# Performance work log

Hardware: AMD Instinct MI355X
Metric: run time of the kernel (lower is better)

The kernel has to match this reference:

```python
import jax, jax.numpy as jnp
import numpy as np

S = 2048          # total tokens (prefill, batch folded into seq dim)
H = 32            # num query heads
HKV = 8           # num kv heads (GQA)
G = H // HKV      # query heads per kv head
D = 128           # head_dim
SCALE = D ** -0.5 # flex_attention default scale
DIFF_BS = 32      # diffusion block size for the block mask


def setup_inputs() -> dict:
    key = jax.random.key(0)
    k1, k2, k3 = jax.random.split(key, 3)
    q = jax.random.normal(k1, (S, H * D), dtype=jnp.float32)
    k = jax.random.normal(k2, (S, HKV * D), dtype=jnp.float32)
    v = jax.random.normal(k3, (S, HKV * D), dtype=jnp.float32)
    # diffusion block-causal mask: token i attends to all tokens in diffusion
    # blocks up to and including its own block (matches attn_metadata.block_mask
    # semantics fed into dllm_block_mask / flex_attention)
    blk = jnp.arange(S) // DIFF_BS
    block_mask = blk[:, None] >= blk[None, :]  # [S, S] bool
    return {"q": q, "k": k, "v": v, "block_mask": block_mask}


def reference(q, k, v, block_mask):
    # q: [S, H*D]; k, v: [S, HKV*D]; block_mask: [S, S] bool
    qh = q.reshape(S, HKV, G, D)   # group query heads by shared kv head (enable_gqa)
    kh = k.reshape(S, HKV, D)
    vh = v.reshape(S, HKV, D)
    # scores: [HKV, G, S_q, S_k]
    scores = jnp.einsum('qhgd,khd->hgqk', qh, kh) * SCALE
    neg = jnp.finfo(scores.dtype).min
    scores = jnp.where(block_mask[None, None, :, :], scores, neg)
    p = jax.nn.softmax(scores, axis=-1)
    o = jnp.einsum('hgqk,khd->qhgd', p, vh)  # [S, HKV, G, D]
    # prefill epilogue: rearrange '1 h s d -> s (h d)'
    return o.reshape(S, H * D)
```

## Files before the change

kernel.cpp:

```cpp
#include <hip/hip_runtime.h>
#include <hip/hip_bf16.h>

typedef __attribute__((ext_vector_type(8)))  short short8;
typedef __attribute__((ext_vector_type(16))) float f32x16;
typedef unsigned short u16;
typedef unsigned int   u32;

__device__ __forceinline__ u16 f2b(float f){
    __hip_bfloat16 h = __float2bfloat16(f);
    u16 u; __builtin_memcpy(&u, &h, 2); return u;
}
__device__ __forceinline__ u32 pk2(float lo, float hi){
    return (u32)f2b(lo) | ((u32)f2b(hi) << 16);
}
__device__ __forceinline__ float b2f(u16 u){
    u32 w = ((u32)u) << 16; float f; __builtin_memcpy(&f, &w, 4); return f;
}

#define PART_STRIDE 8448

template<bool SPLIT>
__global__ __launch_bounds__(256, 2)
void dllm_attn(const float* __restrict__ Qg, const float* __restrict__ Kg,
               const float* __restrict__ Vg, float* __restrict__ Og,
               char* __restrict__ Wg)
{
    __shared__ alignas(16) char kl[64 * 256];
    __shared__ alignas(16) char vl[128 * 128];

    const int bid = blockIdx.x;
    const int kh  = bid & 7;
    int tq, ci, uu = 0;
    if (SPLIT){
        uu = 159 - (bid >> 3);
        if (uu < 16)      { tq = uu; ci = 0; }
        else if (uu < 48) { const int x = uu - 16; tq = 16 + (x >> 1); ci = x & 1; }
        else if (uu < 96) { const int x = uu - 48; const int d3 = x / 3; tq = 32 + d3; ci = x - 3 * d3; }
        else              { const int x = uu - 96; tq = 48 + (x >> 2); ci = x & 3; }
    } else { tq = 63 - (bid >> 3); ci = 0; }
    const int q0   = tq << 5;
    const int nvis = q0 + 32;
    const int ntt  = (tq + 2) >> 1;
    const int t0   = SPLIT ? (ci << 3) : 0;
    const int t1   = SPLIT ? min(t0 + 8, ntt) : ntt;
    const int nch  = SPLIT ? ((tq >> 4) + 1) : 1;

    const int tid = threadIdx.x;
    const int wv  = tid >> 6;
    const int ln  = tid & 63;
    const int lq  = ln & 31;
    const int hi  = ln >> 5;
    const int swz = (ln & 7) << 4;
    const int h   = (kh << 2) + wv;

    const float QS = 0.088388347648318447f * 1.4426950408889634f;
    short8 qf[8];
    {
        const float* qp = Qg + (size_t)(q0 + lq) * 4096 + h * 128 + hi * 8;
        #pragma unroll
        for (int ds = 0; ds < 8; ++ds){
            const float4 a = *reinterpret_cast<const float4*>(qp + ds * 16);
            const float4 b = *reinterpret_cast<const float4*>(qp + ds * 16 + 4);
            qf[ds] = __builtin_bit_cast(short8,
                make_uint4(pk2(a.x * QS, a.y * QS), pk2(a.z * QS, a.w * QS),
                           pk2(b.x * QS, b.y * QS), pk2(b.z * QS, b.w * QS)));
        }
    }

    f32x16 oa[4];
    #pragma unroll
    for (int i = 0; i < 4; ++i)
        #pragma unroll
        for (int j = 0; j < 16; ++j) oa[i][j] = 0.f;
    float mR = -1e30f, lR = 0.f;

    const int sr = tid >> 2;
    const int sc = (tid & 3) << 5;

    for (int t = t0; t < t1; ++t){
        const int kv0 = t << 6;
        const bool full = (kv0 + 64) <= nvis;

        __syncthreads();
        {
            const float* kp = Kg + (size_t)(kv0 + sr) * 1024 + (kh << 7) + sc;
            #pragma unroll
            for (int w = 0; w < 4; ++w){
                const float4 a = *reinterpret_cast<const float4*>(kp + w * 8);
                const float4 b = *reinterpret_cast<const float4*>(kp + w * 8 + 4);
                const uint4 pkd = make_uint4(pk2(a.x,a.y), pk2(a.z,a.w),
                                             pk2(b.x,b.y), pk2(b.z,b.w));
                const int byte = sr * 256 + (((sc << 1) + (w << 4)) ^ ((sr & 7) << 4));
                *reinterpret_cast<uint4*>(&kl[byte]) = pkd;
            }
            const float* vp = Vg + (size_t)(kv0 + sr) * 1024 + (kh << 7) + sc;
            #pragma unroll
            for (int w = 0; w < 8; ++w){
                const float4 a = *reinterpret_cast<const float4*>(vp + w * 4);
                const float vv[4] = {a.x, a.y, a.z, a.w};
                #pragma unroll
                for (int e = 0; e < 4; ++e){
                    const int row = sc + (w << 2) + e;
                    const int byte = (row << 7) + ((sr << 1) ^ ((row & 7) << 4));
                    *reinterpret_cast<u16*>(&vl[byte]) = f2b(vv[e]);
                }
            }
        }
        __syncthreads();

        f32x16 s0, s1;
        #pragma unroll
        for (int i = 0; i < 16; ++i){ s0[i] = 0.f; s1[i] = 0.f; }
        #pragma unroll
        for (int ds = 0; ds < 8; ++ds){
            const short8 a0 = *reinterpret_cast<const short8*>(
                &kl[lq * 256 + (((ds << 5) + (hi << 4)) ^ swz)]);
            s0 = __builtin_amdgcn_mfma_f32_32x32x16_bf16(a0, qf[ds], s0, 0, 0, 0);
        }
        if (full){
            #pragma unroll
            for (int ds = 0; ds < 8; ++ds){
                const short8 a1 = *reinterpret_cast<const short8*>(
                    &kl[(32 + lq) * 256 + (((ds << 5) + (hi << 4)) ^ swz)]);
                s1 = __builtin_amdgcn_mfma_f32_32x32x16_bf16(a1, qf[ds], s1, 0, 0, 0);
            }
        }

        float p0[16], p1[16];
        float mx = -1e30f;
        #pragma unroll
        for (int r = 0; r < 16; ++r){ p0[r] = s0[r]; mx = fmaxf(mx, s0[r]); }
        if (full){
            #pragma unroll
            for (int r = 0; r < 16; ++r){ p1[r] = s1[r]; mx = fmaxf(mx, s1[r]); }
        }
        mx = fmaxf(mx, __shfl_xor(mx, 32, 64));
        const float mn = fmaxf(mR, mx);
        const float cf = __builtin_exp2f(mR - mn);
        mR = mn;
        float ps = 0.f;
        #pragma unroll
        for (int r = 0; r < 16; ++r){ p0[r] = __builtin_exp2f(p0[r] - mn); ps += p0[r]; }
        if (full){
            #pragma unroll
            for (int r = 0; r < 16; ++r){ p1[r] = __builtin_exp2f(p1[r] - mn); ps += p1[r]; }
        }
        ps += __shfl_xor(ps, 32, 64);
        lR = lR * cf + ps;
        #pragma unroll
        for (int i = 0; i < 4; ++i)
            #pragma unroll
            for (int j = 0; j < 16; ++j) oa[i][j] *= cf;

        u32 pw0[8], px0[8], pw1[8], px1[8];
        #pragma unroll
        for (int rr = 0; rr < 8; ++rr){
            pw0[rr] = pk2(p0[2*rr], p0[2*rr+1]);
            px0[rr] = (u32)__shfl_xor((int)pw0[rr], 32, 64);
        }
        if (full){
            #pragma unroll
            for (int rr = 0; rr < 8; ++rr){
                pw1[rr] = pk2(p1[2*rr], p1[2*rr+1]);
                px1[rr] = (u32)__shfl_xor((int)pw1[rr], 32, 64);
            }
        }

        short8 pf[4];
        #pragma unroll
        for (int ks = 0; ks < 4; ++ks){
            if (ks < 2 || full){
                const u32* pwt = (ks >> 1) ? pw1 : pw0;
                const u32* pxt = (ks >> 1) ? px1 : px0;
                u32 wb[4];
                #pragma unroll
                for (int w = 0; w < 4; ++w){
                    const int b = (w & 1) + ((ks & 1) << 2);
                    const u32 own = hi ? pwt[b + 2] : pwt[b];
                    const u32 oth = hi ? pxt[b + 2] : pxt[b];
                    wb[w] = (hi == (w >> 1)) ? own : oth;
                }
                pf[ks] = __builtin_bit_cast(short8, make_uint4(wb[0], wb[1], wb[2], wb[3]));
            }
        }

        #pragma unroll
        for (int dt = 0; dt < 4; ++dt){
            #pragma unroll
            for (int ks = 0; ks < 4; ++ks){
                if (ks < 2 || full){
                    const short8 vf = *reinterpret_cast<const short8*>(
                        &vl[((dt << 5) + lq) * 128 + (((ks << 5) + (hi << 4)) ^ swz)]);
                    oa[dt] = __builtin_amdgcn_mfma_f32_32x32x16_bf16(vf, pf[ks], oa[dt], 0, 0, 0);
                }
            }
        }
    }

    if (!SPLIT || nch == 1){
        const float rl = 1.f / lR;
        float* op = Og + (size_t)(q0 + lq) * 4096 + (h << 7) + (hi << 2);
        #pragma unroll
        for (int dt = 0; dt < 4; ++dt){
            #pragma unroll
            for (int g2 = 0; g2 < 4; ++g2){
                float4 w4;
                w4.x = oa[dt][4*g2 + 0] * rl;
                w4.y = oa[dt][4*g2 + 1] * rl;
                w4.z = oa[dt][4*g2 + 2] * rl;
                w4.w = oa[dt][4*g2 + 3] * rl;
                *reinterpret_cast<float4*>(op + (dt << 5) + (g2 << 3)) = w4;
            }
        }
    } else {
        const int pu = ((kh * 144 + (uu - 16)) << 2) + wv;
        char* base = Wg + (size_t)pu * PART_STRIDE;
        #pragma unroll
        for (int i = 0; i < 8; ++i){
            const int e0 = i * 8;
            uint4 w4;
            w4.x = pk2(oa[(e0+0)>>4][(e0+0)&15], oa[(e0+1)>>4][(e0+1)&15]);
            w4.y = pk2(oa[(e0+2)>>4][(e0+2)&15], oa[(e0+3)>>4][(e0+3)&15]);
            w4.z = pk2(oa[(e0+4)>>4][(e0+4)&15], oa[(e0+5)>>4][(e0+5)&15]);
            w4.w = pk2(oa[(e0+6)>>4][(e0+6)&15], oa[(e0+7)>>4][(e0+7)&15]);
            *reinterpret_cast<uint4*>(base + ln * 128 + i * 16) = w4;
        }
        if (hi == 0){
            *reinterpret_cast<float*>(base + 8192 + lq * 4) = mR;
            *reinterpret_cast<float*>(base + 8320 + lq * 4) = lR;
        }
    }
}

__global__ __launch_bounds__(64, 4)
void dllm_merge(float* __restrict__ Og, const char* __restrict__ Wg)
{
    __shared__ float lds2[32][132];
    const int b  = blockIdx.x;
    const int h  = b & 31;
    const int tq = 16 + (b >> 5);
    const int kh = h >> 2, wv = h & 3;
    const int nch = (tq >> 4) + 1;
    int ub;
    if (tq < 32)      ub = 16 + ((tq - 16) << 1);
    else if (tq < 48) ub = 48 + (tq - 32) * 3;
    else              ub = 96 + ((tq - 48) << 2);

    const int ln = threadIdx.x;
    const int lq = ln & 31, hi = ln >> 5;

    const char* bases[4];
    float mv[4], lv[4];
    float M = -1e30f;
    for (int c = 0; c < 4; ++c){
        if (c < nch){
            bases[c] = Wg + (size_t)(((kh * 144 + (ub - 16 + c)) << 2) + wv) * PART_STRIDE;
            mv[c] = *reinterpret_cast<const float*>(bases[c] + 8192 + lq * 4);
            lv[c] = *reinterpret_cast<const float*>(bases[c] + 8320 + lq * 4);
            M = fmaxf(M, mv[c]);
        }
    }
    float wsum = 0.f;
    float acc[64];
    #pragma unroll
    for (int e = 0; e < 64; ++e) acc[e] = 0.f;
    for (int c = 0; c < 4; ++c){
        if (c < nch){
            const float w = __builtin_exp2f(mv[c] - M);
            wsum += lv[c] * w;
            const uint4* pp = reinterpret_cast<const uint4*>(bases[c] + ln * 128);
            #pragma unroll
            for (int i = 0; i < 8; ++i){
                const uint4 w4 = pp[i];
                const u32 ww[4] = {w4.x, w4.y, w4.z, w4.w};
                #pragma unroll
                for (int k = 0; k < 4; ++k){
                    acc[i*8 + k*2 + 0] += b2f((u16)(ww[k] & 0xffffu)) * w;
                    acc[i*8 + k*2 + 1] += b2f((u16)(ww[k] >> 16)) * w;
                }
            }
        }
    }
    const float rl = 1.f / wsum;
    #pragma unroll
    for (int e = 0; e < 64; ++e){
        const int dt = e >> 4, j = e & 15;
        lds2[lq][dt*32 + (j & 3) + ((j >> 2) << 3) + (hi << 2)] = acc[e] * rl;
    }
    __syncthreads();
    const int q0 = tq << 5;
    #pragma unroll
    for (int it = 0; it < 16; ++it){
        const int idx = it * 64 + ln;
        const int row = idx >> 5;
        const int c4  = idx & 31;
        const float4 v = *reinterpret_cast<const float4*>(&lds2[row][c4 * 4]);
        *reinterpret_cast<float4*>(Og + (size_t)(q0 + row) * 4096 + h * 128 + c4 * 4) = v;
    }
}

extern "C" void kernel_launch(void* const* d_in, const int* in_sizes, int n_in,
                              void* d_out, int out_size, void* d_ws, size_t ws_size,
                              hipStream_t stream) {
    const float* Q = (const float*)d_in[0];
    const float* K = (const float*)d_in[1];
    const float* V = (const float*)d_in[2];
    float* O = (float*)d_out;
    const size_t need = (size_t)4608 * PART_STRIDE;
    if (ws_size >= need){
        dllm_attn<true><<<dim3(1280), dim3(256), 0, stream>>>(Q, K, V, O, (char*)d_ws);
        dllm_merge<<<dim3(1536), dim3(64), 0, stream>>>(O, (const char*)d_ws);
    } else {
        dllm_attn<false><<<dim3(512), dim3(256), 0, stream>>>(Q, K, V, O, (char*)d_ws);
    }
}
```

Measured before the change: 229.7 us.

## Spread merge kernel over 256 threads and write outputs directly without LDS

The split-KV merge kernel now uses 256 threads per block instead of 64. Each thread handles one query row and a 16-column slice, so it keeps 16 accumulators instead of 64. All partial loads are issued up front, and results are stored straight to global memory with float4 writes. This removes the LDS transpose and the barrier, and cuts per-thread register pressure and serial load latency, at the cost of partly coalesced stores (64 bytes per thread per row).

```diff
diff --git a/kernel.cpp b/kernel.cpp
--- a/kernel.cpp
+++ b/kernel.cpp
@@ -232,10 +232,9 @@
     }
 }
 
-__global__ __launch_bounds__(64, 4)
+__global__ __launch_bounds__(256, 2)
 void dllm_merge(float* __restrict__ Og, const char* __restrict__ Wg)
 {
-    __shared__ float lds2[32][132];
     const int b  = blockIdx.x;
     const int h  = b & 31;
     const int tq = 16 + (b >> 5);
@@ -246,56 +245,61 @@
     else if (tq < 48) ub = 48 + (tq - 32) * 3;
     else              ub = 96 + ((tq - 48) << 2);
 
-    const int ln = threadIdx.x;
-    const int lq = ln & 31, hi = ln >> 5;
+    const int tid = threadIdx.x;
+    const int q   = tid >> 3;
+    const int s   = tid & 7;
 
     const char* bases[4];
     float mv[4], lv[4];
     float M = -1e30f;
+    #pragma unroll
     for (int c = 0; c < 4; ++c){
         if (c < nch){
             bases[c] = Wg + (size_t)(((kh * 144 + (ub - 16 + c)) << 2) + wv) * PART_STRIDE;
-            mv[c] = *reinterpret_cast<const float*>(bases[c] + 8192 + lq * 4);
-            lv[c] = *reinterpret_cast<const float*>(bases[c] + 8320 + lq * 4);
+            mv[c] = *reinterpret_cast<const float*>(bases[c] + 8192 + q * 4);
+            lv[c] = *reinterpret_cast<const float*>(bases[c] + 8320 + q * 4);
             M = fmaxf(M, mv[c]);
         }
     }
+    uint4 wlo[4], whi[4];
+    #pragma unroll
+    for (int c = 0; c < 4; ++c){
+        if (c < nch){
+            wlo[c] = *reinterpret_cast<const uint4*>(bases[c] + q * 128 + s * 16);
+            whi[c] = *reinterpret_cast<const uint4*>(bases[c] + (q + 32) * 128 + s * 16);
+        }
+    }
     float wsum = 0.f;
-    float acc[64];
-    #pragma unroll
-    for (int e = 0; e < 64; ++e) acc[e] = 0.f;
+    float acc[16];
+    #pragma unroll
+    for (int e = 0; e < 16; ++e) acc[e] = 0.f;
+    #pragma unroll
     for (int c = 0; c < 4; ++c){
         if (c < nch){
             const float w = __builtin_exp2f(mv[c] - M);
             wsum += lv[c] * w;
-            const uint4* pp = reinterpret_cast<const uint4*>(bases[c] + ln * 128);
-            #pragma unroll
-            for (int i = 0; i < 8; ++i){
-                const uint4 w4 = pp[i];
-                const u32 ww[4] = {w4.x, w4.y, w4.z, w4.w};
-                #pragma unroll
-                for (int k = 0; k < 4; ++k){
-                    acc[i*8 + k*2 + 0] += b2f((u16)(ww[k] & 0xffffu)) * w;
-                    acc[i*8 + k*2 + 1] += b2f((u16)(ww[k] >> 16)) * w;
-                }
+            const u32 wl[4] = {wlo[c].x, wlo[c].y, wlo[c].z, wlo[c].w};
+            const u32 wh[4] = {whi[c].x, whi[c].y, whi[c].z, whi[c].w};
+            #pragma unroll
+            for (int k = 0; k < 4; ++k){
+                const int dl = ((k & 1) << 1) + ((k >> 1) << 3);
+                acc[dl + 0] += b2f((u16)(wl[k] & 0xffffu)) * w;
+                acc[dl + 1] += b2f((u16)(wl[k] >> 16)) * w;
+                acc[dl + 4] += b2f((u16)(wh[k] & 0xffffu)) * w;
+                acc[dl + 5] += b2f((u16)(wh[k] >> 16)) * w;
             }
         }
     }
     const float rl = 1.f / wsum;
-    #pragma unroll
-    for (int e = 0; e < 64; ++e){
-        const int dt = e >> 4, j = e & 15;
-        lds2[lq][dt*32 + (j & 3) + ((j >> 2) << 3) + (hi << 2)] = acc[e] * rl;
-    }
-    __syncthreads();
-    const int q0 = tq << 5;
-    #pragma unroll
-    for (int it = 0; it < 16; ++it){
-        const int idx = it * 64 + ln;
-        const int row = idx >> 5;
-        const int c4  = idx & 31;
-        const float4 v = *reinterpret_cast<const float4*>(&lds2[row][c4 * 4]);
-        *reinterpret_cast<float4*>(Og + (size_t)(q0 + row) * 4096 + h * 128 + c4 * 4) = v;
+    float* op = Og + (size_t)((tq << 5) + q) * 4096 + h * 128 + (s << 4);
+    #pragma unroll
+    for (int g = 0; g < 4; ++g){
+        float4 v4;
+        v4.x = acc[g*4 + 0] * rl;
+        v4.y = acc[g*4 + 1] * rl;
+        v4.z = acc[g*4 + 2] * rl;
+        v4.w = acc[g*4 + 3] * rl;
+        *reinterpret_cast<float4*>(op + (g << 2)) = v4;
     }
 }
 
@@ -309,7 +313,7 @@
     const size_t need = (size_t)4608 * PART_STRIDE;
     if (ws_size >= need){
         dllm_attn<true><<<dim3(1280), dim3(256), 0, stream>>>(Q, K, V, O, (char*)d_ws);
-        dllm_merge<<<dim3(1536), dim3(64), 0, stream>>>(O, (const char*)d_ws);
+        dllm_merge<<<dim3(1536), dim3(256), 0, stream>>>(O, (const char*)d_ws);
     } else {
         dllm_attn<false><<<dim3(512), dim3(256), 0, stream>>>(Q, K, V, O, (char*)d_ws);
     }
```

Result: no change. 228.2 us (-0.7%).
